# Performance work log

Hardware: AMD Instinct MI355X
Metric: run time of the kernel (lower is better)

Reference implementation:

```python
import jax, jax.numpy as jnp
import numpy as np

DIRECTIONS = [(0, 0), (1, 0), (-1, 0), (0, 1), (0, -1)]  # (dx, dy)
BN_EPS = 1e-5


def shift2d(x, directions=DIRECTIONS):
    # x: (B, C, H, W). Split channels into G groups, roll each spatially,
    # zero out the wrapped-around border (zero_pad mode), then concat.
    C = x.shape[1]
    G = len(directions)
    base = C // G
    sizes = [base] * (G - 1) + [C - base * (G - 1)]
    starts = np.concatenate([[0], np.cumsum(sizes)])
    out = []
    for i, (dx, dy) in enumerate(directions):
        chunk = x[:, starts[i]:starts[i + 1]]
        if dx == 0 and dy == 0:
            out.append(chunk)
            continue
        y = jnp.roll(chunk, shift=(dy, dx), axis=(-2, -1))
        if dy > 0:
            y = y.at[..., :dy, :].set(0.0)
        elif dy < 0:
            y = y.at[..., dy:, :].set(0.0)
        if dx > 0:
            y = y.at[..., :, :dx].set(0.0)
        elif dx < 0:
            y = y.at[..., :, dx:].set(0.0)
        out.append(y)
    return jnp.concatenate(out, axis=1)


def setup_inputs() -> dict:
    key = jax.random.key(0)
    k1, k2, k3, k4 = jax.random.split(key, 4)
    B, Cin, Cout, H, W = 32, 256, 256, 56, 56
    x = jax.random.normal(k1, (B, Cin, H, W), dtype=jnp.float32)
    pw_w = jax.random.normal(k2, (Cout, Cin), dtype=jnp.float32) * (1.0 / np.sqrt(Cin))
    gamma = jnp.ones((Cout,), dtype=jnp.float32)
    beta = jnp.zeros((Cout,), dtype=jnp.float32)
    running_mean = jax.random.normal(k3, (Cout,), dtype=jnp.float32) * 0.1
    running_var = jax.random.uniform(k4, (Cout,), dtype=jnp.float32, minval=0.5, maxval=1.5)
    return {"x": x, "pw_w": pw_w, "gamma": gamma, "beta": beta,
            "running_mean": running_mean, "running_var": running_var}


def reference(x, pw_w, gamma, beta, running_mean, running_var):
    # Shift (parameter-free spatial mixing)
    y = shift2d(x)
    # stride=1 -> down is Identity
    # 1x1 conv (no bias): pointwise channel mixing
    y = jnp.einsum('bchw,oc->bohw', y, pw_w)
    # BatchNorm2d (inference form with running stats) + ReLU
    inv = gamma * jax.lax.rsqrt(running_var + BN_EPS)
    y = y * inv[None, :, None, None] + (beta - running_mean * inv)[None, :, None, None]
    return jax.nn.relu(y)
```

## Files before the change

kernel.cpp:

```cpp
#include <hip/hip_runtime.h>

#define H_ 56
#define W_ 56
#define HW_ 3136
#define CIN_ 256
#define COUT_ 256

typedef __attribute__((ext_vector_type(8))) short short8;
typedef __attribute__((ext_vector_type(4))) float f32x4;

__device__ __forceinline__ int swz(int n) { return ((n ^ (n >> 3)) & 7) << 3; }

__device__ __forceinline__ unsigned short f2bf(float f) {
  union { float f; unsigned int i; } v; v.f = f;
  unsigned int b = v.i + (0x7fffu + ((v.i >> 16) & 1u));
  return (unsigned short)(b >> 16);
}

__global__ __launch_bounds__(256, 2)
void shiftconv_gemm(const float* __restrict__ x,
                    const float* __restrict__ wgt,
                    const float* __restrict__ gamma,
                    const float* __restrict__ beta,
                    const float* __restrict__ rmean,
                    const float* __restrict__ rvar,
                    float* __restrict__ out)
{
  __shared__ unsigned short Alds[128 * 64];
  __shared__ unsigned short Blds[128 * 64];
  __shared__ float bnp[256];

  const int t    = threadIdx.x;
  const int bn   = blockIdx.x;
  const int bm   = blockIdx.y;
  const int lane = t & 63;
  const int wv   = t >> 6;
  const int wm   = wv >> 1;
  const int wn   = wv & 1;
  const int quad = lane >> 4;
  const int l15  = lane & 15;

  if (t < 128) {
    int o = bm * 128 + t;
    float inv = gamma[o] * rsqrtf(rvar[o] + 1e-5f);
    bnp[2 * t]     = inv;
    bnp[2 * t + 1] = beta[o] - rmean[o] * inv;
  }

  const int chunk  = t & 15;
  const int krow   = t >> 4;
  const int nloc0  = chunk * 8;
  const int nglob0 = bn * 128 + nloc0;
  const int bidx   = nglob0 / HW_;
  const int rem    = nglob0 - bidx * HW_;
  const int hh     = rem / W_;
  const int w0     = rem - hh * W_;
  const size_t xb  = (size_t)bidx * CIN_ * HW_;

  const int kc  = t & 7;
  const int am0 = t >> 3;

  f32x4 acc[4][4];
  #pragma unroll
  for (int i = 0; i < 4; ++i)
    #pragma unroll
    for (int j = 0; j < 4; ++j)
      acc[i][j] = (f32x4){0.f, 0.f, 0.f, 0.f};

  for (int k0 = 0; k0 < CIN_; k0 += 64) {
    #pragma unroll
    for (int p = 0; p < 4; ++p) {
      int m = am0 + 32 * p;
      int o = bm * 128 + m;
      const float* src = wgt + (size_t)o * CIN_ + k0 + kc * 8;
      float4 f0 = *(const float4*)(src);
      float4 f1 = *(const float4*)(src + 4);
      union { uint4 v; unsigned short s[8]; } pk;
      pk.s[0] = f2bf(f0.x); pk.s[1] = f2bf(f0.y);
      pk.s[2] = f2bf(f0.z); pk.s[3] = f2bf(f0.w);
      pk.s[4] = f2bf(f1.x); pk.s[5] = f2bf(f1.y);
      pk.s[6] = f2bf(f1.z); pk.s[7] = f2bf(f1.w);
      *(uint4*)(&Alds[m * 64 + ((kc * 8) ^ swz(m))]) = pk.v;
    }
    #pragma unroll
    for (int p = 0; p < 4; ++p) {
      int kk = krow + 16 * p;
      int c  = k0 + kk;
      int dx, dy;
      if (c < 102)      { if (c < 51) { dx = 0; dy = 0; } else { dx = 1; dy = 0; } }
      else if (c < 153) { dx = -1; dy = 0; }
      else if (c < 204) { dx = 0;  dy = 1; }
      else              { dx = 0;  dy = -1; }
      int h2 = hh - dy;
      float vals[8];
      if ((unsigned)h2 < (unsigned)H_) {
        const float* row = x + xb + (size_t)c * HW_ + h2 * W_;
        float4 a = *(const float4*)(row + w0);
        float4 b = *(const float4*)(row + w0 + 4);
        float s[8] = {a.x, a.y, a.z, a.w, b.x, b.y, b.z, b.w};
        if (dx == 0) {
          #pragma unroll
          for (int i = 0; i < 8; ++i) vals[i] = s[i];
        } else if (dx == 1) {
          #pragma unroll
          for (int i = 7; i >= 1; --i) vals[i] = s[i - 1];
          vals[0] = (w0 > 0) ? row[w0 - 1] : 0.0f;
        } else {
          #pragma unroll
          for (int i = 0; i < 7; ++i) vals[i] = s[i + 1];
          vals[7] = (w0 + 8 < W_) ? row[w0 + 8] : 0.0f;
        }
      } else {
        #pragma unroll
        for (int i = 0; i < 8; ++i) vals[i] = 0.0f;
      }
      #pragma unroll
      for (int i = 0; i < 8; ++i) {
        int nl = nloc0 + i;
        Blds[nl * 64 + (kk ^ swz(nl))] = f2bf(vals[i]);
      }
    }
    __syncthreads();
    #pragma unroll
    for (int ks = 0; ks < 2; ++ks) {
      int kb = ks * 32 + quad * 8;
      short8 af[4], bf[4];
      #pragma unroll
      for (int f = 0; f < 4; ++f) {
        int ml = wm * 64 + f * 16 + l15;
        af[f] = *(const short8*)(&Alds[ml * 64 + (kb ^ swz(ml))]);
        int nl = wn * 64 + f * 16 + l15;
        bf[f] = *(const short8*)(&Blds[nl * 64 + (kb ^ swz(nl))]);
      }
      #pragma unroll
      for (int mf = 0; mf < 4; ++mf)
        #pragma unroll
        for (int nf = 0; nf < 4; ++nf)
          acc[mf][nf] = __builtin_amdgcn_mfma_f32_16x16x32_bf16(
              af[mf], bf[nf], acc[mf][nf], 0, 0, 0);
    }
    __syncthreads();
  }

  size_t nbase[4];
  #pragma unroll
  for (int nf = 0; nf < 4; ++nf) {
    int ng  = bn * 128 + wn * 64 + nf * 16 + l15;
    int b2  = ng / HW_;
    int hw2 = ng - b2 * HW_;
    nbase[nf] = (size_t)b2 * COUT_ * HW_ + hw2;
  }
  #pragma unroll
  for (int mf = 0; mf < 4; ++mf) {
    int mloc = wm * 64 + mf * 16 + quad * 4;
    float inv[4], add[4];
    #pragma unroll
    for (int r = 0; r < 4; ++r) {
      inv[r] = bnp[2 * (mloc + r)];
      add[r] = bnp[2 * (mloc + r) + 1];
    }
    size_t obase = (size_t)(bm * 128 + mloc) * HW_;
    #pragma unroll
    for (int nf = 0; nf < 4; ++nf) {
      #pragma unroll
      for (int r = 0; r < 4; ++r) {
        float v = acc[mf][nf][r] * inv[r] + add[r];
        out[nbase[nf] + obase + (size_t)r * HW_] = fmaxf(v, 0.0f);
      }
    }
  }
}

extern "C" void kernel_launch(void* const* d_in, const int* in_sizes, int n_in,
                              void* d_out, int out_size, void* d_ws, size_t ws_size,
                              hipStream_t stream) {
  const float* x     = (const float*)d_in[0];
  const float* wgt   = (const float*)d_in[1];
  const float* gamma = (const float*)d_in[2];
  const float* beta  = (const float*)d_in[3];
  const float* rmean = (const float*)d_in[4];
  const float* rvar  = (const float*)d_in[5];
  float* out = (float*)d_out;
  dim3 grid(784, 2);
  shiftconv_gemm<<<grid, dim3(256), 0, stream>>>(x, wgt, gamma, beta, rmean, rvar, out);
}
```

Baseline: 219.7 us.

## Pre-convert weights to bf16 and double-buffer K-loop with direct-to-LDS loads

A separate prep kernel converts the weights to bf16 once per call into a swizzled global buffer. The GEMM then streams weight tiles straight into LDS with global_load_lds and double-buffers both A and B over a K step of 32. The next x tile is loaded from global memory while the current MFMAs run. The N tile is halved to 64 and occupancy is raised to 4 blocks per CU, which doubles the number of blocks and the redundant weight-tile reads, and adds a second kernel launch.

```diff
diff --git a/kernel.cpp b/kernel.cpp
--- a/kernel.cpp
+++ b/kernel.cpp
@@ -9,7 +9,9 @@
 typedef __attribute__((ext_vector_type(8))) short short8;
 typedef __attribute__((ext_vector_type(4))) float f32x4;
 
-__device__ __forceinline__ int swz(int n) { return ((n ^ (n >> 3)) & 7) << 3; }
+__device__ unsigned short g_wbf[COUT_ * CIN_];
+
+__device__ __forceinline__ int swz32(int n) { return ((n ^ (n >> 3)) & 3) << 3; }
 
 __device__ __forceinline__ unsigned short f2bf(float f) {
   union { float f; unsigned int i; } v; v.f = f;
@@ -17,17 +19,83 @@
   return (unsigned short)(b >> 16);
 }
 
-__global__ __launch_bounds__(256, 2)
+__device__ __forceinline__ void gload_lds16(const unsigned short* g, unsigned short* l) {
+  __builtin_amdgcn_global_load_lds(
+      (const __attribute__((address_space(1))) unsigned int*)g,
+      (__attribute__((address_space(3))) unsigned int*)l, 16, 0, 0);
+}
+
+__device__ __forceinline__ void shift_decode(int c, int& dx, int& dy) {
+  if (c < 102)      { dy = 0; dx = (c < 51) ? 0 : 1; }
+  else if (c < 153) { dx = -1; dy = 0; }
+  else if (c < 204) { dx = 0;  dy = 1; }
+  else              { dx = 0;  dy = -1; }
+}
+
+__global__ __launch_bounds__(256)
+void prep_weights(const float* __restrict__ wgt) {
+  int idx  = blockIdx.x * 256 + threadIdx.x;
+  int tile = idx >> 12;
+  int bm = tile >> 3, kt = tile & 7;
+  int e   = idx & 4095;
+  int m   = e >> 5, col = e & 31;
+  int o   = bm * 128 + m;
+  int k   = kt * 32 + (col ^ swz32(m));
+  g_wbf[idx] = f2bf(wgt[o * CIN_ + k]);
+}
+
+__device__ __forceinline__ void load_x(const float* __restrict__ x, size_t xb,
+                                       int hh, int w0, int c,
+                                       float4& p0, float4& p1, float& pe) {
+  int dx, dy; shift_decode(c, dx, dy);
+  int h2 = hh - dy;
+  p0 = make_float4(0.f, 0.f, 0.f, 0.f);
+  p1 = make_float4(0.f, 0.f, 0.f, 0.f);
+  pe = 0.f;
+  if ((unsigned)h2 < (unsigned)H_) {
+    const float* row = x + xb + (size_t)c * HW_ + h2 * W_;
+    p0 = *(const float4*)(row + w0);
+    p1 = *(const float4*)(row + w0 + 4);
+    if (dx == 1)       { if (w0 > 0)      pe = row[w0 - 1]; }
+    else if (dx == -1) { if (w0 + 8 < W_) pe = row[w0 + 8]; }
+  }
+}
+
+__device__ __forceinline__ void write_b(unsigned short* __restrict__ B,
+                                        int nloc0, int krow, int c,
+                                        const float4& p0, const float4& p1, float pe) {
+  int dx, dy; shift_decode(c, dx, dy);
+  float s[8] = {p0.x, p0.y, p0.z, p0.w, p1.x, p1.y, p1.z, p1.w};
+  float vals[8];
+  if (dx == 0) {
+    #pragma unroll
+    for (int i = 0; i < 8; ++i) vals[i] = s[i];
+  } else if (dx == 1) {
+    #pragma unroll
+    for (int i = 7; i >= 1; --i) vals[i] = s[i - 1];
+    vals[0] = pe;
+  } else {
+    #pragma unroll
+    for (int i = 0; i < 7; ++i) vals[i] = s[i + 1];
+    vals[7] = pe;
+  }
+  #pragma unroll
+  for (int i = 0; i < 8; ++i) {
+    int nl = nloc0 + i;
+    B[nl * 32 + (krow ^ swz32(nl))] = f2bf(vals[i]);
+  }
+}
+
+__global__ __launch_bounds__(256, 4)
 void shiftconv_gemm(const float* __restrict__ x,
-                    const float* __restrict__ wgt,
                     const float* __restrict__ gamma,
                     const float* __restrict__ beta,
                     const float* __restrict__ rmean,
                     const float* __restrict__ rvar,
                     float* __restrict__ out)
 {
-  __shared__ unsigned short Alds[128 * 64];
-  __shared__ unsigned short Blds[128 * 64];
+  __shared__ unsigned short Alds[2][128 * 32];
+  __shared__ unsigned short Blds[2][64 * 32];
   __shared__ float bnp[256];
 
   const int t    = threadIdx.x;
@@ -47,105 +115,77 @@
     bnp[2 * t + 1] = beta[o] - rmean[o] * inv;
   }
 
-  const int chunk  = t & 15;
-  const int krow   = t >> 4;
+  const int chunk  = t & 7;
+  const int krow   = t >> 3;
   const int nloc0  = chunk * 8;
-  const int nglob0 = bn * 128 + nloc0;
+  const int nglob0 = bn * 64 + nloc0;
   const int bidx   = nglob0 / HW_;
   const int rem    = nglob0 - bidx * HW_;
   const int hh     = rem / W_;
   const int w0     = rem - hh * W_;
   const size_t xb  = (size_t)bidx * CIN_ * HW_;
 
-  const int kc  = t & 7;
-  const int am0 = t >> 3;
-
-  f32x4 acc[4][4];
+  const unsigned short* wsrc = g_wbf + bm * (8 * 4096) + t * 8;
+
+  f32x4 acc[4][2];
   #pragma unroll
   for (int i = 0; i < 4; ++i)
     #pragma unroll
-    for (int j = 0; j < 4; ++j)
+    for (int j = 0; j < 2; ++j)
       acc[i][j] = (f32x4){0.f, 0.f, 0.f, 0.f};
 
-  for (int k0 = 0; k0 < CIN_; k0 += 64) {
-    #pragma unroll
-    for (int p = 0; p < 4; ++p) {
-      int m = am0 + 32 * p;
-      int o = bm * 128 + m;
-      const float* src = wgt + (size_t)o * CIN_ + k0 + kc * 8;
-      float4 f0 = *(const float4*)(src);
-      float4 f1 = *(const float4*)(src + 4);
-      union { uint4 v; unsigned short s[8]; } pk;
-      pk.s[0] = f2bf(f0.x); pk.s[1] = f2bf(f0.y);
-      pk.s[2] = f2bf(f0.z); pk.s[3] = f2bf(f0.w);
-      pk.s[4] = f2bf(f1.x); pk.s[5] = f2bf(f1.y);
-      pk.s[6] = f2bf(f1.z); pk.s[7] = f2bf(f1.w);
-      *(uint4*)(&Alds[m * 64 + ((kc * 8) ^ swz(m))]) = pk.v;
-    }
-    #pragma unroll
-    for (int p = 0; p < 4; ++p) {
-      int kk = krow + 16 * p;
-      int c  = k0 + kk;
-      int dx, dy;
-      if (c < 102)      { if (c < 51) { dx = 0; dy = 0; } else { dx = 1; dy = 0; } }
-      else if (c < 153) { dx = -1; dy = 0; }
-      else if (c < 204) { dx = 0;  dy = 1; }
-      else              { dx = 0;  dy = -1; }
-      int h2 = hh - dy;
-      float vals[8];
-      if ((unsigned)h2 < (unsigned)H_) {
-        const float* row = x + xb + (size_t)c * HW_ + h2 * W_;
-        float4 a = *(const float4*)(row + w0);
-        float4 b = *(const float4*)(row + w0 + 4);
-        float s[8] = {a.x, a.y, a.z, a.w, b.x, b.y, b.z, b.w};
-        if (dx == 0) {
-          #pragma unroll
-          for (int i = 0; i < 8; ++i) vals[i] = s[i];
-        } else if (dx == 1) {
-          #pragma unroll
-          for (int i = 7; i >= 1; --i) vals[i] = s[i - 1];
-          vals[0] = (w0 > 0) ? row[w0 - 1] : 0.0f;
-        } else {
-          #pragma unroll
-          for (int i = 0; i < 7; ++i) vals[i] = s[i + 1];
-          vals[7] = (w0 + 8 < W_) ? row[w0 + 8] : 0.0f;
-        }
-      } else {
-        #pragma unroll
-        for (int i = 0; i < 8; ++i) vals[i] = 0.0f;
-      }
+  float4 p0, p1;
+  float  pe;
+
+  {
+    const unsigned short* g = wsrc;
+    gload_lds16(g,        &Alds[0][wv * 512]);
+    gload_lds16(g + 2048, &Alds[0][wv * 512 + 2048]);
+  }
+  load_x(x, xb, hh, w0, krow, p0, p1, pe);
+  write_b(&Blds[0][0], nloc0, krow, krow, p0, p1, pe);
+  __syncthreads();
+
+  const int kb = quad * 8;
+  int buf = 0;
+
+  for (int kt = 0; kt < 8; ++kt) {
+    if (kt < 7) {
+      const unsigned short* g = wsrc + (kt + 1) * 4096;
+      gload_lds16(g,        &Alds[buf ^ 1][wv * 512]);
+      gload_lds16(g + 2048, &Alds[buf ^ 1][wv * 512 + 2048]);
+      load_x(x, xb, hh, w0, (kt + 1) * 32 + krow, p0, p1, pe);
+    }
+
+    short8 af[4], bfr[2];
+    #pragma unroll
+    for (int f = 0; f < 4; ++f) {
+      int ml = wm * 64 + f * 16 + l15;
+      af[f] = *(const short8*)(&Alds[buf][ml * 32 + (kb ^ swz32(ml))]);
+    }
+    #pragma unroll
+    for (int g2 = 0; g2 < 2; ++g2) {
+      int nl = wn * 32 + g2 * 16 + l15;
+      bfr[g2] = *(const short8*)(&Blds[buf][nl * 32 + (kb ^ swz32(nl))]);
+    }
+    #pragma unroll
+    for (int mf = 0; mf < 4; ++mf)
       #pragma unroll
-      for (int i = 0; i < 8; ++i) {
-        int nl = nloc0 + i;
-        Blds[nl * 64 + (kk ^ swz(nl))] = f2bf(vals[i]);
-      }
-    }
+      for (int nf = 0; nf < 2; ++nf)
+        acc[mf][nf] = __builtin_amdgcn_mfma_f32_16x16x32_bf16(
+            af[mf], bfr[nf], acc[mf][nf], 0, 0, 0);
+
+    if (kt < 7)
+      write_b(&Blds[buf ^ 1][0], nloc0, krow, (kt + 1) * 32 + krow, p0, p1, pe);
+
     __syncthreads();
-    #pragma unroll
-    for (int ks = 0; ks < 2; ++ks) {
-      int kb = ks * 32 + quad * 8;
-      short8 af[4], bf[4];
-      #pragma unroll
-      for (int f = 0; f < 4; ++f) {
-        int ml = wm * 64 + f * 16 + l15;
-        af[f] = *(const short8*)(&Alds[ml * 64 + (kb ^ swz(ml))]);
-        int nl = wn * 64 + f * 16 + l15;
-        bf[f] = *(const short8*)(&Blds[nl * 64 + (kb ^ swz(nl))]);
-      }
-      #pragma unroll
-      for (int mf = 0; mf < 4; ++mf)
-        #pragma unroll
-        for (int nf = 0; nf < 4; ++nf)
-          acc[mf][nf] = __builtin_amdgcn_mfma_f32_16x16x32_bf16(
-              af[mf], bf[nf], acc[mf][nf], 0, 0, 0);
-    }
-    __syncthreads();
-  }
-
-  size_t nbase[4];
-  #pragma unroll
-  for (int nf = 0; nf < 4; ++nf) {
-    int ng  = bn * 128 + wn * 64 + nf * 16 + l15;
+    buf ^= 1;
+  }
+
+  size_t nbase[2];
+  #pragma unroll
+  for (int nf = 0; nf < 2; ++nf) {
+    int ng  = bn * 64 + wn * 32 + nf * 16 + l15;
     int b2  = ng / HW_;
     int hw2 = ng - b2 * HW_;
     nbase[nf] = (size_t)b2 * COUT_ * HW_ + hw2;
@@ -161,10 +201,10 @@
     }
     size_t obase = (size_t)(bm * 128 + mloc) * HW_;
     #pragma unroll
-    for (int nf = 0; nf < 4; ++nf) {
+    for (int nf = 0; nf < 2; ++nf) {
       #pragma unroll
       for (int r = 0; r < 4; ++r) {
-        float v = acc[mf][nf][r] * inv[r] + add[r];
+        float v = fmaf(acc[mf][nf][r], inv[r], add[r]);
         out[nbase[nf] + obase + (size_t)r * HW_] = fmaxf(v, 0.0f);
       }
     }
@@ -181,6 +221,7 @@
   const float* rmean = (const float*)d_in[4];
   const float* rvar  = (const float*)d_in[5];
   float* out = (float*)d_out;
-  dim3 grid(784, 2);
-  shiftconv_gemm<<<grid, dim3(256), 0, stream>>>(x, wgt, gamma, beta, rmean, rvar, out);
-}
+
+  prep_weights<<<dim3(256), dim3(256), 0, stream>>>(wgt);
+  shiftconv_gemm<<<dim3(1568, 2), dim3(256), 0, stream>>>(x, gamma, beta, rmean, rvar, out);
+}
```

After: 211.4 us. 3.8% less time.
